# Performance work log

Measured on AMD Instinct MI355X. Metric: run time of the kernel, lower is better.

Reference implementation:

```python
import jax, jax.numpy as jnp
import numpy as np

B, T, Rn, D, O, E, H, C, TM = 20, 20, 20, 4096, 16, 512, 8, 68, 1900


def l2norm(x, axis=-1, eps=1e-12):
    return x / jnp.maximum(jnp.linalg.norm(x, axis=axis, keepdims=True), eps)


def setup_inputs() -> dict:
    key = jax.random.key(0)
    ks = jax.random.split(key, 10)
    return {
        "features": jax.random.normal(ks[0], (B, T, Rn, D), jnp.float32),
        "labels": jax.random.randint(ks[1], (B, O), 0, C),
        "temporal_mem": jax.random.normal(ks[2], (TM, T, D), jnp.float32),
        "entity_W": jax.random.normal(ks[3], (C, E), jnp.float32) / np.float32(np.sqrt(C)),
        "entity_b": jnp.zeros((E,), jnp.float32),
        "Wq": jax.random.normal(ks[4], (E, E), jnp.float32) / np.float32(np.sqrt(E)),
        "Wk": jax.random.normal(ks[5], (D, E), jnp.float32) / np.float32(np.sqrt(D)),
        "Wv": jax.random.normal(ks[6], (D, E), jnp.float32) / np.float32(np.sqrt(D)),
        "Wo": jax.random.normal(ks[7], (E, E), jnp.float32) / np.float32(np.sqrt(E)),
        "obj_W1": jax.random.normal(ks[8], (D, E), jnp.float32) / np.float32(np.sqrt(D)),
        "obj_b1": jnp.zeros((E,), jnp.float32),
        "obj_W2": jax.random.normal(ks[9], (E, 1), jnp.float32) / np.float32(np.sqrt(E)),
        "obj_b2": jnp.zeros((1,), jnp.float32),
    }


def reference(features, labels, temporal_mem, entity_W, entity_b, Wq, Wk, Wv, Wo,
              obj_W1, obj_b1, obj_W2, obj_b2):
    beta = 0.5   # loss mixing weight (module's beta)
    qgce = 0.7   # generalized-CE exponent
    Dh = E // H
    # region features, L2-normalized (dataset_feat == 'CVPR' path)
    Rf = l2norm(features)                                   # [B,T,Rn,D]

    # ---- temporal memory-bank kNN retrieval ----
    R_max = l2norm(jnp.max(Rf, axis=2))                     # [B,T,D] max-pool over regions
    mem_max = l2norm(jnp.max(temporal_mem, axis=1))         # [TM,D] max-pool over frames
    sim = jnp.einsum('btd,md->btm', R_max, mem_max)         # [B,T,TM]
    idx = jnp.argmax(sim, axis=-1)                          # [B,T] nearest memory slot
    Rp = temporal_mem[idx]                                  # [B,T,T,D] gathered memory videos
    mem_feat = jnp.max(Rp, axis=2)                          # [B,T,D]

    # ---- entity (object-label) embedding: one-hot with class 0 zeroed ----
    onehot = jax.nn.one_hot(labels, C, dtype=features.dtype)
    onehot = onehot * (labels != 0)[..., None].astype(features.dtype)
    Qe = onehot @ entity_W + entity_b                       # [B,O,E]

    # ---- multi-head attention fusion over regions + retrieved memory ----
    kv = jnp.concatenate([Rf.reshape(B, T * Rn, D), mem_feat], axis=1)  # [B,N,D]
    q = (Qe @ Wq).reshape(B, O, H, Dh)
    k = (kv @ Wk).reshape(B, -1, H, Dh)
    v = (kv @ Wv).reshape(B, -1, H, Dh)
    scores = jnp.einsum('bohd,bnhd->bhon', q, k) / np.float32(np.sqrt(Dh))
    attn = jax.nn.softmax(scores, axis=-1)
    fused = jnp.einsum('bhon,bnhd->bohd', attn, v).reshape(B, O, E) @ Wo  # [B,O,E]

    # ---- top-k region objectness selection + generalized CE ----
    QR = jax.lax.stop_gradient(jnp.mean(scores, axis=1)[:, :, :T * Rn].reshape(B, O, T, Rn))
    hi = jnp.argmax(QR, axis=-1)                            # [B,O,T] top-1 region
    lo = jnp.argmin(QR, axis=-1)                            # [B,O,T] low region
    bidx = jnp.arange(B)[:, None, None]
    tidx = jnp.arange(T)[None, None, :]
    R_high = Rf[bidx, tidx, hi]                             # [B,O,T,D]
    R_low = Rf[bidx, tidx, lo]                              # [B,O,T,D]
    osel = (labels != 0).astype(features.dtype)             # [B,O]
    onum = jnp.maximum(jnp.sum(osel, axis=1), 1.0)
    mlp = lambda x: jax.nn.sigmoid(jnp.tanh(x @ obj_W1 + obj_b1) @ obj_W2 + obj_b2)
    s_hi = mlp(R_high * osel[..., None, None]).squeeze(-1)  # [B,O,T]
    s_lo = mlp(R_low * osel[..., None, None]).squeeze(-1)
    gce_hi = jnp.mean((1.0 - (s_hi + 1e-7) ** qgce) / qgce * osel[..., None], axis=-1)
    gce_lo = jnp.mean((1.0 - (1.0 - s_lo + 1e-7) ** qgce) / qgce * osel[..., None], axis=-1)
    gce = jnp.mean(jnp.sum(gce_hi, axis=1) / onum) + jnp.mean(jnp.sum(gce_lo, axis=1) / onum)

    return fused + beta * gce
```

## Files before the change

kernel.cpp:

```cpp
#include <hip/hip_runtime.h>

#define B_   20
#define T_   20
#define RN   20
#define D_   4096
#define O_   16
#define E_   512
#define H_   8
#define DH   64
#define TM_  1900
#define MREG 8192
#define NW   1536
#define NSIM 2048
#define MSIM 512
#define CAP  256

using f32x4  = __attribute__((ext_vector_type(4))) float;
using bf16x8 = __attribute__((ext_vector_type(8))) __bf16;

__device__ __forceinline__ unsigned short f2bf(float f){
  unsigned u = __float_as_uint(f);
  u += 0x7fffu + ((u >> 16) & 1u);
  return (unsigned short)(u >> 16);
}

__device__ __forceinline__ void st_bf4(unsigned short* dst, float4 v){
  ushort4 o = make_ushort4(f2bf(v.x), f2bf(v.y), f2bf(v.z), f2bf(v.w));
  *(ushort4*)dst = o;
}

__device__ __forceinline__ float bsum256(float v, float* sh){
  int t = threadIdx.x;
  for (int o = 32; o; o >>= 1) v += __shfl_down(v, o, 64);
  __syncthreads();
  if ((t & 63) == 0) sh[t >> 6] = v;
  __syncthreads();
  return sh[0] + sh[1] + sh[2] + sh[3];
}

__device__ __forceinline__ float bmax256(float v, float* sh){
  int t = threadIdx.x;
  for (int o = 32; o; o >>= 1) v = fmaxf(v, __shfl_down(v, o, 64));
  __syncthreads();
  if ((t & 63) == 0) sh[t >> 6] = v;
  __syncthreads();
  return fmaxf(fmaxf(sh[0], sh[1]), fmaxf(sh[2], sh[3]));
}

__device__ __forceinline__ void gld16(const void* g, void* l){
  __builtin_amdgcn_global_load_lds(
      (const __attribute__((address_space(1))) unsigned int*)g,
      (__attribute__((address_space(3))) unsigned int*)l, 16, 0, 0);
}

__global__ __launch_bounds__(256) void k_pre(
    const float* __restrict__ F, const float* __restrict__ TMm,
    const float* __restrict__ Wk, const float* __restrict__ Wv, const float* __restrict__ W1,
    unsigned short* __restrict__ Wall,
    unsigned short* __restrict__ A, float* __restrict__ rmaxr, float* __restrict__ rmsum,
    unsigned short* __restrict__ ubf,
    float* __restrict__ umax, float* __restrict__ msum, unsigned short* __restrict__ gbf,
    const int* __restrict__ labels, const float* __restrict__ entW, const float* __restrict__ entB,
    const float* __restrict__ Wq, float* __restrict__ q){
  __shared__ char smem[4352];
  int bid = blockIdx.x, t = threadIdx.x;
  if (bid < 2048){
    int m = bid;
    if (m >= TM_){
      int4 zz = make_int4(0,0,0,0);
      int4* r2 = (int4*)(gbf + (size_t)m*D_);
      r2[t] = zz; r2[t + 256] = zz;
      return;
    }
    float* sh = (float*)smem;
    const float* base = TMm + (size_t)m*T_*D_;
    float4 mx[4];
#pragma unroll
    for (int i = 0; i < 4; ++i) mx[i] = make_float4(-1e30f,-1e30f,-1e30f,-1e30f);
    float4 va[2][4];
#pragma unroll
    for (int i = 0; i < 4; ++i) va[0][i] = *(const float4*)(base + i*1024 + t*4);
#pragma unroll
    for (int f = 0; f < T_; ++f){
      int c = f & 1;
      if (f + 1 < T_){
#pragma unroll
        for (int i = 0; i < 4; ++i)
          va[c^1][i] = *(const float4*)(base + (size_t)(f+1)*D_ + i*1024 + t*4);
      }
#pragma unroll
      for (int i = 0; i < 4; ++i){
        mx[i].x = fmaxf(mx[i].x, va[c][i].x); mx[i].y = fmaxf(mx[i].y, va[c][i].y);
        mx[i].z = fmaxf(mx[i].z, va[c][i].z); mx[i].w = fmaxf(mx[i].w, va[c][i].w);
      }
    }
    float s = 0.f;
#pragma unroll
    for (int i = 0; i < 4; ++i){
      *(float4*)(umax + (size_t)m*D_ + i*1024 + t*4) = mx[i];
      st_bf4(gbf + (size_t)m*D_ + i*1024 + t*4, mx[i]);
      s += mx[i].x*mx[i].x + mx[i].y*mx[i].y + mx[i].z*mx[i].z + mx[i].w*mx[i].w;
    }
    s = bsum256(s, sh);
    if (t == 0) msum[m] = s;
  } else if (bid < 2560){
    int bt = bid - 2048;
    if (bt >= 400){
      int4 zz = make_int4(0,0,0,0);
      int4* r1 = (int4*)(ubf + (size_t)bt*D_);
      r1[t] = zz; r1[t + 256] = zz;
      int base = 8000 + (bt - 400)*2;
#pragma unroll
      for (int k = 0; k < 2; ++k){
        if (base + k < MREG){
          int4* r2 = (int4*)(A + (size_t)(base + k)*D_);
          r2[t] = zz; r2[t + 256] = zz;
        }
      }
      return;
    }
    float* sh = (float*)smem;
    const float* fb = F + (size_t)bt*RN*D_;
    unsigned short* ab = A + (size_t)bt*RN*D_;
    float4 mx[4];
#pragma unroll
    for (int i = 0; i < 4; ++i) mx[i] = make_float4(-1e30f,-1e30f,-1e30f,-1e30f);
    float4 vn[4];
#pragma unroll
    for (int i = 0; i < 4; ++i) vn[i] = *(const float4*)(fb + i*1024 + t*4);
    for (int r = 0; r < RN; ++r){
      float4 v[4];
      float s = 0.f;
#pragma unroll
      for (int i = 0; i < 4; ++i){
        v[i] = vn[i];
        s += v[i].x*v[i].x + v[i].y*v[i].y + v[i].z*v[i].z + v[i].w*v[i].w;
      }
      if (r + 1 < RN){
#pragma unroll
        for (int i = 0; i < 4; ++i)
          vn[i] = *(const float4*)(fb + (size_t)(r+1)*D_ + i*1024 + t*4);
      }
      s = bsum256(s, sh);
      float ri = 1.f / fmaxf(sqrtf(s), 1e-12f);
#pragma unroll
      for (int i = 0; i < 4; ++i){
        v[i].x *= ri; v[i].y *= ri; v[i].z *= ri; v[i].w *= ri;
        st_bf4(ab + (size_t)r*D_ + i*1024 + t*4, v[i]);
        mx[i].x = fmaxf(mx[i].x, v[i].x); mx[i].y = fmaxf(mx[i].y, v[i].y);
        mx[i].z = fmaxf(mx[i].z, v[i].z); mx[i].w = fmaxf(mx[i].w, v[i].w);
      }
    }
    float s2 = 0.f;
#pragma unroll
    for (int i = 0; i < 4; ++i){
      *(float4*)(rmaxr + (size_t)bt*D_ + i*1024 + t*4) = mx[i];
      s2 += mx[i].x*mx[i].x + mx[i].y*mx[i].y + mx[i].z*mx[i].z + mx[i].w*mx[i].w;
    }
    s2 = bsum256(s2, sh);
    if (t == 0) rmsum[bt] = s2;
    float inv = 1.f / fmaxf(sqrtf(s2), 1e-12f);
#pragma unroll
    for (int i = 0; i < 4; ++i){
      float4 u = mx[i];
      u.x *= inv; u.y *= inv; u.z *= inv; u.w *= inv;
      st_bf4(ubf + (size_t)bt*D_ + i*1024 + t*4, u);
    }
  } else if (bid < 8704){
    int wti = bid - 2560;
    float* tile = (float*)smem;
    int kb = (wti & 127) * 32, nb = (wti >> 7) * 32;
    const float* src; int nc0;
    if (nb < 512)      { src = Wk; nc0 = nb; }
    else if (nb < 1024){ src = Wv; nc0 = nb - 512; }
    else               { src = W1; nc0 = nb - 1024; }
    int tx = t & 31, ty = t >> 5;
#pragma unroll
    for (int j = 0; j < 4; ++j){
      int k = kb + ty + j*8;
      tile[(ty + j*8)*33 + tx] = src[(size_t)k*E_ + nc0 + tx];
    }
    __syncthreads();
#pragma unroll
    for (int j = 0; j < 4; ++j){
      int n = nb + ty + j*8;
      int k = kb + tx;
      Wall[(size_t)n*D_ + k] = f2bf(tile[tx*33 + ty + j*8]);
    }
  } else {
    int bo = bid - 8704;
    float* qe = (float*)smem;
    int lab = labels[bo];
    float sel = (lab != 0) ? 1.f : 0.f;
    qe[t]       = sel * entW[(size_t)lab*E_ + t]       + entB[t];
    qe[t + 256] = sel * entW[(size_t)lab*E_ + t + 256] + entB[t + 256];
    __syncthreads();
    float a0 = 0.f, a1 = 0.f;
    for (int ep = 0; ep < E_; ++ep){
      float r = qe[ep];
      a0 += r * Wq[(size_t)ep*E_ + t];
      a1 += r * Wq[(size_t)ep*E_ + t + 256];
    }
    q[(size_t)bo*E_ + t] = a0;
    q[(size_t)bo*E_ + t + 256] = a1;
  }
}

__global__ __launch_bounds__(512, 1) void k_gemm3(
    const unsigned short* __restrict__ Akv, const unsigned short* __restrict__ Wall,
    const unsigned short* __restrict__ ubf, const unsigned short* __restrict__ gbf,
    float* __restrict__ C2, float* __restrict__ simc, float* __restrict__ Gc){
  __shared__ char lds[131072];
  int bid = blockIdx.x;
  bid = (bid & 7)*32 + (bid >> 3);
  const unsigned short *A, *Bw; float* C; int nNt, ldc, mt, nt;
  if (bid < 192){       A = Akv; Bw = Wall;  C = C2;   nNt = 6; ldc = NW;   mt = bid/6;  nt = bid%6; }
  else if (bid < 208){  int s = bid - 192;
                        A = ubf; Bw = gbf;   C = simc; nNt = 8; ldc = NSIM; mt = s/8;    nt = s%8; }
  else {                int s = bid - 208;
                        A = gbf; Bw = Wall;  C = Gc;   nNt = 6; ldc = NW;   mt = s/6;    nt = s%6; }
  int tid = threadIdx.x, wid = tid >> 6, l = tid & 63;
  int wr = (wid >> 2) * 128;
  int wc = (wid & 3) * 64;
  int fr = l & 15, fq = l >> 4;
  const char* Ab = (const char*)A + (size_t)mt*256*(size_t)(D_*2);
  const char* Bb = (const char*)Bw + (size_t)nt*256*(size_t)(D_*2);
  f32x4 acc[8][4];
#pragma unroll
  for (int m = 0; m < 8; ++m)
#pragma unroll
    for (int n = 0; n < 4; ++n) acc[m][n] = (f32x4){0.f,0.f,0.f,0.f};

#pragma unroll
  for (int i = 0; i < 4; ++i){
    int idx = i*512 + tid;
    int row = idx >> 3, u = idx & 7;
    int ul = u ^ (row & 7);
    gld16(Ab + (size_t)row*(D_*2) + (size_t)(ul*16), lds + idx*16);
    gld16(Bb + (size_t)row*(D_*2) + (size_t)(ul*16), lds + 32768 + idx*16);
  }
  __syncthreads();

  int c = 0;
  for (int kt = 0; kt < D_/64; ++kt){
    if (kt < D_/64 - 1){
      int ktoff = (kt + 1) * 128;
      char* dA = lds + (c^1)*65536;
      char* dB = dA + 32768;
#pragma unroll
      for (int i = 0; i < 4; ++i){
        int idx = i*512 + tid;
        int row = idx >> 3, u = idx & 7;
        int ul = u ^ (row & 7);
        gld16(Ab + (size_t)row*(D_*2) + ktoff + ul*16, dA + idx*16);
        gld16(Bb + (size_t)row*(D_*2) + ktoff + ul*16, dB + idx*16);
      }
    }
    const char* LA = lds + c*65536;
    const char* LB = LA + 32768;
    bf16x8 bv[4][2];
#pragma unroll
    for (int n = 0; n < 4; ++n)
#pragma unroll
      for (int kk = 0; kk < 2; ++kk){
        int row = wc + n*16 + fr;
        int u = (kk*4 + fq) ^ (row & 7);
        bv[n][kk] = *(const bf16x8*)(LB + row*128 + u*16);
      }
    __builtin_amdgcn_s_setprio(1);
#pragma unroll
    for (int mp = 0; mp < 4; ++mp){
      bf16x8 av[2][2];
#pragma unroll
      for (int mm = 0; mm < 2; ++mm)
#pragma unroll
        for (int kk = 0; kk < 2; ++kk){
          int row = wr + (mp*2 + mm)*16 + fr;
          int u = (kk*4 + fq) ^ (row & 7);
          av[mm][kk] = *(const bf16x8*)(LA + row*128 + u*16);
        }
#pragma unroll
      for (int mm = 0; mm < 2; ++mm)
#pragma unroll
        for (int n = 0; n < 4; ++n)
#pragma unroll
          for (int kk = 0; kk < 2; ++kk)
            acc[mp*2 + mm][n] = __builtin_amdgcn_mfma_f32_16x16x32_bf16(
                av[mm][kk], bv[n][kk], acc[mp*2 + mm][n], 0, 0, 0);
    }
    __builtin_amdgcn_s_setprio(0);
    __syncthreads();
    c ^= 1;
  }
  size_t crow0 = (size_t)mt*256 + wr, ccol0 = (size_t)nt*256 + wc;
#pragma unroll
  for (int m = 0; m < 8; ++m)
#pragma unroll
    for (int n = 0; n < 4; ++n){
      size_t r0 = crow0 + m*16 + fq*4, c0 = ccol0 + n*16 + fr;
#pragma unroll
      for (int j = 0; j < 4; ++j)
        C[(r0 + j)*(size_t)ldc + c0] = acc[m][n][j];
    }
}

__global__ __launch_bounds__(256) void k_pick(const float* __restrict__ simc,
                                              const float* __restrict__ rmaxr, const float* __restrict__ rmsum,
                                              const float* __restrict__ umax, const float* __restrict__ msum,
                                              const float* __restrict__ Gc, float* __restrict__ C2){
  int bt = blockIdx.x, t = threadIdx.x;
  __shared__ float srow[1920];
  __shared__ float sh[4];
  __shared__ int cnt;
  __shared__ int cl[CAP];
  for (int m = t; m < TM_; m += 256)
    srow[m] = simc[(size_t)bt*NSIM + m] * (1.f / fmaxf(sqrtf(msum[m]), 1e-12f));
  if (t == 0) cnt = 0;
  __syncthreads();
  float mx = -1e30f;
  for (int m = t; m < TM_; m += 256) mx = fmaxf(mx, srow[m]);
  mx = bmax256(mx, sh);
  float thr = mx - 2.5e-4f;
  for (int m = t; m < TM_; m += 256){
    if (srow[m] >= thr){
      int p = atomicAdd(&cnt, 1);
      if (p < CAP) cl[p] = m;
    }
  }
  __syncthreads();
  int cn = cnt < CAP ? cnt : CAP;
  float rinvv = 1.f / fmaxf(sqrtf(rmsum[bt]), 1e-12f);
  const float* a = rmaxr + (size_t)bt*D_;
  float best = -1e30f; int bestm = 0x7fffffff;
  for (int ci = 0; ci < cn; ++ci){
    int m = cl[ci];
    const float* wrow = umax + (size_t)m*D_;
    float p = 0.f;
    for (int i = t*4; i < D_; i += 1024){
      float4 av = *(const float4*)(a + i);
      float4 wv = *(const float4*)(wrow + i);
      p += av.x*wv.x + av.y*wv.y + av.z*wv.z + av.w*wv.w;
    }
    p = bsum256(p, sh);
    float sim = p * rinvv * (1.f / fmaxf(sqrtf(msum[m]), 1e-12f));
    if (sim > best || (sim == best && m < bestm)){ best = sim; bestm = m; }
  }
  const float4* src = (const float4*)(Gc + (size_t)bestm*NW);
  float4* dst = (float4*)(C2 + (size_t)(MREG + bt)*NW);
  if (t < 128){ dst[t] = src[t]; dst[t + 128] = src[t + 128]; dst[t + 256] = src[t + 256]; }
}

__global__ __launch_bounds__(256) void k_post(const float* __restrict__ q, const float* __restrict__ c2,
                                              float* __restrict__ fpre, int* __restrict__ hi,
                                              int* __restrict__ lo, const float* __restrict__ b1,
                                              const float* __restrict__ W2, const float* __restrict__ b2,
                                              float* __restrict__ z){
  __shared__ char smem[58368];
  int bid = blockIdx.x, t = threadIdx.x;
  if (bid < 160){
    int b = bid >> 3, h = bid & 7;
    int w = t >> 6, l = t & 63;
    float* qhp = (float*)smem;
    float* kb  = (float*)(smem + 4160);
    float* sc  = (float*)(smem + 31460);
    for (int i = t; i < O_*DH; i += 256){
      int o = i >> 6, d = i & 63;
      qhp[o*65 + d] = q[((size_t)(b*O_ + o))*E_ + h*DH + d] * 0.125f;
    }
    __syncthreads();
    for (int c = 0; c < 4; ++c){
      for (int i = t; i < 105*DH; i += 256){
        int j = i >> 6, d = i & 63;
        int n = c*105 + j;
        size_t row = n < 400 ? (size_t)b*400 + n : (size_t)MREG + b*20 + (n - 400);
        kb[j*65 + d] = c2[row*NW + h*DH + d];
      }
      __syncthreads();
      for (int i = t; i < O_*105; i += 256){
        int o = i / 105, j = i % 105;
        float acc = 0.f;
        for (int d = 0; d < DH; ++d) acc += qhp[o*65 + d] * kb[j*65 + d];
        sc[o*420 + c*105 + j] = acc;
      }
      __syncthreads();
    }
    for (int oi = 0; oi < 4; ++oi){
      int o = w + oi*4;
      float mxv = -1e30f;
      for (int n = l; n < 420; n += 64) mxv = fmaxf(mxv, sc[o*420 + n]);
      for (int of = 32; of; of >>= 1) mxv = fmaxf(mxv, __shfl_xor(mxv, of, 64));
      float sum = 0.f;
      for (int n = l; n < 420; n += 64){ float e = expf(sc[o*420 + n] - mxv); sc[o*420 + n] = e; sum += e; }
      for (int of = 32; of; of >>= 1) sum += __shfl_xor(sum, of, 64);
      float inv = 1.f / sum;
      for (int n = l; n < 420; n += 64) sc[o*420 + n] *= inv;
    }
    __syncthreads();
    float acc[4] = {0.f, 0.f, 0.f, 0.f};
    for (int c = 0; c < 4; ++c){
      for (int i = t; i < 105*DH; i += 256){
        int j = i >> 6, d = i & 63;
        int n = c*105 + j;
        size_t row = n < 400 ? (size_t)b*400 + n : (size_t)MREG + b*20 + (n - 400);
        kb[j*65 + d] = c2[row*NW + E_ + h*DH + d];
      }
      __syncthreads();
#pragma unroll
      for (int og = 0; og < 4; ++og){
        int o = og*4 + w;
        float a = 0.f;
        for (int j = 0; j < 105; ++j) a += sc[o*420 + c*105 + j] * kb[j*65 + l];
        acc[og] += a;
      }
      __syncthreads();
    }
#pragma unroll
    for (int og = 0; og < 4; ++og){
      int o = og*4 + w;
      fpre[((size_t)(b*O_ + o))*E_ + h*DH + l] = acc[og];
    }
  } else if (bid < 560){
    int bt = bid - 160;
    int b = bt / T_, tt = bt % T_;
    float* kl = (float*)smem;
    float* qr = (float*)(smem + 41040);
    for (int i = t; i < RN*E_; i += 256){
      int r = i >> 9, e = i & 511;
      kl[r*513 + e] = c2[((size_t)b*400 + tt*RN + r)*NW + e];
    }
    __syncthreads();
#pragma unroll
    for (int pp = 0; pp < 2; ++pp){
      int p = t + pp*256;
      if (p < O_*RN){
        int o = p / RN, r = p % RN;
        const float* qrow = q + ((size_t)(b*O_ + o))*E_;
        float acc = 0.f;
        for (int e = 0; e < E_; ++e) acc += qrow[e] * kl[r*513 + e];
        qr[o*20 + r] = acc;
      }
    }
    __syncthreads();
    if (t < O_){
      int o = t;
      float bh = qr[o*20], bl = qr[o*20]; int ih = 0, il = 0;
#pragma unroll
      for (int r = 1; r < RN; ++r){
        float v = qr[o*20 + r];
        if (v > bh){ bh = v; ih = r; }
        if (v < bl){ bl = v; il = r; }
      }
      int rowbase = b*400 + tt*RN;
      int outi = (b*O_ + o)*T_ + tt;
      hi[outi] = rowbase + ih;
      lo[outi] = rowbase + il;
    }
  } else {
    int g = (bid - 560)*4 + (t >> 6);
    int l = t & 63;
    const float* hrow = c2 + (size_t)g*NW + 1024;
    float acc = 0.f;
    for (int e = l; e < E_; e += 64) acc += tanhf(hrow[e] + b1[e]) * W2[e];
    for (int of = 32; of; of >>= 1) acc += __shfl_down(acc, of, 64);
    if (l == 0) z[g] = 1.f / (1.f + expf(-(acc + b2[0])));
  }
}

__global__ __launch_bounds__(256) void k_outg(const float* __restrict__ fpre, const float* __restrict__ Wo,
                                              const float* __restrict__ z, const int* __restrict__ hi,
                                              const int* __restrict__ lo, const int* __restrict__ labels,
                                              float* __restrict__ out){
  int bo = blockIdx.x, t = threadIdx.x;
  __shared__ float rowv[E_];
  __shared__ float vb[B_];
  __shared__ int cb[B_];
  __shared__ float gsh;
  rowv[t] = fpre[(size_t)bo*E_ + t];
  rowv[t + 256] = fpre[(size_t)bo*E_ + t + 256];
  if (t < B_){ vb[t] = 0.f; cb[t] = 0; }
  __syncthreads();
  for (int p = t; p < B_*O_; p += 256){
    int b = p / O_;
    if (labels[p] != 0){
      float acc = 0.f;
      for (int tt = 0; tt < T_; ++tt){
        float shi = z[hi[p*T_ + tt]];
        float slo = z[lo[p*T_ + tt]];
        acc += (1.f - __powf(shi + 1e-7f, 0.7f)) / 0.7f;
        acc += (1.f - __powf(1.f - slo + 1e-7f, 0.7f)) / 0.7f;
      }
      atomicAdd(&vb[b], acc / (float)T_);
      atomicAdd(&cb[b], 1);
    }
  }
  __syncthreads();
  if (t == 0){
    float g = 0.f;
    for (int b = 0; b < B_; ++b) g += vb[b] / fmaxf((float)cb[b], 1.f);
    gsh = 0.5f * (g / (float)B_);
  }
  __syncthreads();
  float g = gsh;
  float a0 = 0.f, a1 = 0.f;
  for (int ep = 0; ep < E_; ++ep){
    float r = rowv[ep];
    a0 += r * Wo[(size_t)ep*E_ + t];
    a1 += r * Wo[(size_t)ep*E_ + t + 256];
  }
  out[(size_t)bo*E_ + t] = a0 + g;
  out[(size_t)bo*E_ + t + 256] = a1 + g;
}

extern "C" void kernel_launch(void* const* d_in, const int* in_sizes, int n_in,
                              void* d_out, int out_size, void* d_ws, size_t ws_size,
                              hipStream_t stream) {
  (void)in_sizes; (void)n_in; (void)out_size; (void)ws_size;
  const float* F    = (const float*)d_in[0];
  const int*   labels = (const int*)d_in[1];
  const float* TMm  = (const float*)d_in[2];
  const float* entW = (const float*)d_in[3];
  const float* entB = (const float*)d_in[4];
  const float* Wq   = (const float*)d_in[5];
  const float* Wk   = (const float*)d_in[6];
  const float* Wv   = (const float*)d_in[7];
  const float* Wo   = (const float*)d_in[8];
  const float* W1   = (const float*)d_in[9];
  const float* b1   = (const float*)d_in[10];
  const float* W2   = (const float*)d_in[11];
  const float* b2   = (const float*)d_in[12];
  float* out = (float*)d_out;

  size_t off = 0;
  char* wsb = (char*)d_ws;
  auto alloc = [&](size_t bytes) -> char* {
    char* p = wsb + off; off += (bytes + 255) & ~(size_t)255; return p;
  };
  unsigned short* A_kv = (unsigned short*)alloc((size_t)MREG * D_ * 2);
  unsigned short* Wall = (unsigned short*)alloc((size_t)NW * D_ * 2);
  float* umax          = (float*)alloc((size_t)TM_ * D_ * 4);
  unsigned short* gbf  = (unsigned short*)alloc((size_t)NSIM * D_ * 2);
  unsigned short* ubf  = (unsigned short*)alloc((size_t)MSIM * D_ * 2);
  float* rmaxr = (float*)alloc((size_t)400 * D_ * 4);
  float* simc  = (float*)alloc((size_t)MSIM * NSIM * 4);
  float* Gc    = (float*)alloc((size_t)NSIM * NW * 4);
  float* C2    = (float*)alloc((size_t)(MREG + 512) * NW * 4);
  float* qbuf  = (float*)alloc((size_t)B_ * O_ * E_ * 4);
  float* fpre  = (float*)alloc((size_t)B_ * O_ * E_ * 4);
  float* rmsum = (float*)alloc(400 * 4);
  float* msum  = (float*)alloc(TM_ * 4);
  int*   hib   = (int*)alloc(6400 * 4);
  int*   lob   = (int*)alloc(6400 * 4);
  float* zbuf  = (float*)alloc(8000 * 4);

  k_pre<<<9024, 256, 0, stream>>>(F, TMm, Wk, Wv, W1, Wall, A_kv, rmaxr, rmsum, ubf,
                                  umax, msum, gbf, labels, entW, entB, Wq, qbuf);
  k_gemm3<<<256, 512, 0, stream>>>(A_kv, Wall, ubf, gbf, C2, simc, Gc);
  k_pick<<<400, 256, 0, stream>>>(simc, rmaxr, rmsum, umax, msum, Gc, C2);
  k_post<<<2560, 256, 0, stream>>>(qbuf, C2, fpre, hib, lob, b1, W2, b2, zbuf);
  k_outg<<<B_*O_, 256, 0, stream>>>(fpre, Wo, zbuf, hib, lob, labels, out);
}
```

Before: 487.0 us.

## Interleave next-tile global loads with MFMA phases in the GEMM main loop

Restructures the double-buffered bf16 GEMM loop so the prefetch of the next K tile is split into four quarter-stages, each issued alongside one of the four MFMA sub-phases. It replaces the single end-of-iteration __syncthreads with explicit vmcnt/lgkmcnt waits, s_barrier calls and sched_barriers around each phase. The aim is to spread memory issue across the compute and keep waves in lockstep so loads overlap with matrix math. In exchange it adds more barriers per iteration, and the hand-written waitcnt counts must match the number of outstanding loads exactly to avoid races.

```diff
diff --git a/kernel.cpp b/kernel.cpp
--- a/kernel.cpp
+++ b/kernel.cpp
@@ -231,66 +231,68 @@
 #pragma unroll
     for (int n = 0; n < 4; ++n) acc[m][n] = (f32x4){0.f,0.f,0.f,0.f};
 
-#pragma unroll
-  for (int i = 0; i < 4; ++i){
-    int idx = i*512 + tid;
-    int row = idx >> 3, u = idx & 7;
-    int ul = u ^ (row & 7);
-    gld16(Ab + (size_t)row*(D_*2) + (size_t)(ul*16), lds + idx*16);
-    gld16(Bb + (size_t)row*(D_*2) + (size_t)(ul*16), lds + 32768 + idx*16);
-  }
-  __syncthreads();
-
-  int c = 0;
+  auto stage_half = [&](char* dstbuf, int ktoff, int h){
+    const char* src = (h < 2) ? Ab : Bb;
+    int hh = h & 1;
+    char* dst = dstbuf + ((h < 2) ? 0 : 32768);
+#pragma unroll
+    for (int j = 0; j < 2; ++j){
+      int idx = (2*hh + j)*512 + tid;
+      int row = idx >> 3, u = idx & 7;
+      int ul = u ^ (row & 7);
+      gld16(src + (size_t)row*(size_t)(D_*2) + ktoff + ul*16, dst + idx*16);
+    }
+  };
+
+#pragma unroll
+  for (int h = 0; h < 4; ++h) stage_half(lds, 0, h);
+
   for (int kt = 0; kt < D_/64; ++kt){
-    if (kt < D_/64 - 1){
-      int ktoff = (kt + 1) * 128;
-      char* dA = lds + (c^1)*65536;
-      char* dB = dA + 32768;
-#pragma unroll
-      for (int i = 0; i < 4; ++i){
-        int idx = i*512 + tid;
-        int row = idx >> 3, u = idx & 7;
-        int ul = u ^ (row & 7);
-        gld16(Ab + (size_t)row*(D_*2) + ktoff + ul*16, dA + idx*16);
-        gld16(Bb + (size_t)row*(D_*2) + ktoff + ul*16, dB + idx*16);
-      }
-    }
-    const char* LA = lds + c*65536;
-    const char* LB = LA + 32768;
+    char* curb = lds + (kt & 1)*65536;
+    char* nxtb = lds + ((kt & 1)^1)*65536;
+    int nktoff = (kt + 1)*128;
     bf16x8 bv[4][2];
 #pragma unroll
-    for (int n = 0; n < 4; ++n)
-#pragma unroll
-      for (int kk = 0; kk < 2; ++kk){
-        int row = wc + n*16 + fr;
-        int u = (kk*4 + fq) ^ (row & 7);
-        bv[n][kk] = *(const bf16x8*)(LB + row*128 + u*16);
-      }
-    __builtin_amdgcn_s_setprio(1);
-#pragma unroll
-    for (int mp = 0; mp < 4; ++mp){
+    for (int p = 0; p < 4; ++p){
+      if (kt < D_/64 - 1) stage_half(nxtb, nktoff, p);
+      if (p == 0){
+        if (kt < D_/64 - 1) asm volatile("s_waitcnt vmcnt(2)" ::: "memory");
+        else                asm volatile("s_waitcnt vmcnt(0)" ::: "memory");
+        __builtin_amdgcn_s_barrier();
+        __builtin_amdgcn_sched_barrier(0);
+#pragma unroll
+        for (int n = 0; n < 4; ++n)
+#pragma unroll
+          for (int kk = 0; kk < 2; ++kk){
+            int row = wc + n*16 + fr;
+            int u = (kk*4 + fq) ^ (row & 7);
+            bv[n][kk] = *(const bf16x8*)(curb + 32768 + row*128 + u*16);
+          }
+      }
       bf16x8 av[2][2];
 #pragma unroll
       for (int mm = 0; mm < 2; ++mm)
 #pragma unroll
         for (int kk = 0; kk < 2; ++kk){
-          int row = wr + (mp*2 + mm)*16 + fr;
+          int row = wr + (p*2 + mm)*16 + fr;
           int u = (kk*4 + fq) ^ (row & 7);
-          av[mm][kk] = *(const bf16x8*)(LA + row*128 + u*16);
+          av[mm][kk] = *(const bf16x8*)(curb + row*128 + u*16);
         }
+      __builtin_amdgcn_s_barrier();
+      asm volatile("s_waitcnt lgkmcnt(0)" ::: "memory");
+      __builtin_amdgcn_sched_barrier(0);
+      __builtin_amdgcn_s_setprio(1);
 #pragma unroll
       for (int mm = 0; mm < 2; ++mm)
 #pragma unroll
         for (int n = 0; n < 4; ++n)
 #pragma unroll
           for (int kk = 0; kk < 2; ++kk)
-            acc[mp*2 + mm][n] = __builtin_amdgcn_mfma_f32_16x16x32_bf16(
-                av[mm][kk], bv[n][kk], acc[mp*2 + mm][n], 0, 0, 0);
-    }
-    __builtin_amdgcn_s_setprio(0);
-    __syncthreads();
-    c ^= 1;
+            acc[p*2 + mm][n] = __builtin_amdgcn_mfma_f32_16x16x32_bf16(
+                av[mm][kk], bv[n][kk], acc[p*2 + mm][n], 0, 0, 0);
+      __builtin_amdgcn_s_setprio(0);
+      __builtin_amdgcn_s_barrier();
+    }
   }
   size_t crow0 = (size_t)mt*256 + wr, ccol0 = (size_t)nt*256 + wc;
 #pragma unroll
```

After: 488.4 us. About the same (+0.3%).

## Overlap memory-bank max-pool with main GEMM and split-K the sim/Gc GEMMs

Applied to the files above, without the earlier changes.

Moves the temporal-memory max-pool out of the preprocessing kernel and runs it in the same launch as the main K/V/W1 GEMM tiles, so the bandwidth-bound reduction can overlap with the compute-bound GEMM. The similarity and memory-projection GEMMs move into a separate kernel and use split-K (8 and 4 partitions). This fills more blocks and shortens the serial K loop, and the picking kernel sums the partials. The Gc projection shrinks to 1024 columns. The cost is more partial-sum traffic and an extra launch.

```diff
diff --git a/kernel.cpp b/kernel.cpp
--- a/kernel.cpp
+++ b/kernel.cpp
@@ -13,7 +13,10 @@
 #define NW   1536
 #define NSIM 2048
 #define MSIM 512
+#define NG   1024
 #define CAP  256
+#define SIMK 8
+#define GK   4
 
 using f32x4  = __attribute__((ext_vector_type(4))) float;
 using bf16x8 = __attribute__((ext_vector_type(8))) __bf16;
@@ -53,58 +56,18 @@
       (__attribute__((address_space(3))) unsigned int*)l, 16, 0, 0);
 }
 
-__global__ __launch_bounds__(256) void k_pre(
-    const float* __restrict__ F, const float* __restrict__ TMm,
+__global__ __launch_bounds__(256) void k_prelight(
+    const float* __restrict__ F,
     const float* __restrict__ Wk, const float* __restrict__ Wv, const float* __restrict__ W1,
     unsigned short* __restrict__ Wall,
     unsigned short* __restrict__ A, float* __restrict__ rmaxr, float* __restrict__ rmsum,
     unsigned short* __restrict__ ubf,
-    float* __restrict__ umax, float* __restrict__ msum, unsigned short* __restrict__ gbf,
     const int* __restrict__ labels, const float* __restrict__ entW, const float* __restrict__ entB,
     const float* __restrict__ Wq, float* __restrict__ q){
   __shared__ char smem[4352];
   int bid = blockIdx.x, t = threadIdx.x;
-  if (bid < 2048){
-    int m = bid;
-    if (m >= TM_){
-      int4 zz = make_int4(0,0,0,0);
-      int4* r2 = (int4*)(gbf + (size_t)m*D_);
-      r2[t] = zz; r2[t + 256] = zz;
-      return;
-    }
-    float* sh = (float*)smem;
-    const float* base = TMm + (size_t)m*T_*D_;
-    float4 mx[4];
-#pragma unroll
-    for (int i = 0; i < 4; ++i) mx[i] = make_float4(-1e30f,-1e30f,-1e30f,-1e30f);
-    float4 va[2][4];
-#pragma unroll
-    for (int i = 0; i < 4; ++i) va[0][i] = *(const float4*)(base + i*1024 + t*4);
-#pragma unroll
-    for (int f = 0; f < T_; ++f){
-      int c = f & 1;
-      if (f + 1 < T_){
-#pragma unroll
-        for (int i = 0; i < 4; ++i)
-          va[c^1][i] = *(const float4*)(base + (size_t)(f+1)*D_ + i*1024 + t*4);
-      }
-#pragma unroll
-      for (int i = 0; i < 4; ++i){
-        mx[i].x = fmaxf(mx[i].x, va[c][i].x); mx[i].y = fmaxf(mx[i].y, va[c][i].y);
-        mx[i].z = fmaxf(mx[i].z, va[c][i].z); mx[i].w = fmaxf(mx[i].w, va[c][i].w);
-      }
-    }
-    float s = 0.f;
-#pragma unroll
-    for (int i = 0; i < 4; ++i){
-      *(float4*)(umax + (size_t)m*D_ + i*1024 + t*4) = mx[i];
-      st_bf4(gbf + (size_t)m*D_ + i*1024 + t*4, mx[i]);
-      s += mx[i].x*mx[i].x + mx[i].y*mx[i].y + mx[i].z*mx[i].z + mx[i].w*mx[i].w;
-    }
-    s = bsum256(s, sh);
-    if (t == 0) msum[m] = s;
-  } else if (bid < 2560){
-    int bt = bid - 2048;
+  if (bid < 512){
+    int bt = bid;
     if (bt >= 400){
       int4 zz = make_int4(0,0,0,0);
       int4* r1 = (int4*)(ubf + (size_t)bt*D_);
@@ -166,8 +129,8 @@
       u.x *= inv; u.y *= inv; u.z *= inv; u.w *= inv;
       st_bf4(ubf + (size_t)bt*D_ + i*1024 + t*4, u);
     }
-  } else if (bid < 8704){
-    int wti = bid - 2560;
+  } else if (bid < 6656){
+    int wti = bid - 512;
     float* tile = (float*)smem;
     int kb = (wti & 127) * 32, nb = (wti >> 7) * 32;
     const float* src; int nc0;
@@ -188,7 +151,7 @@
       Wall[(size_t)n*D_ + k] = f2bf(tile[tx*33 + ty + j*8]);
     }
   } else {
-    int bo = bid - 8704;
+    int bo = bid - 6656;
     float* qe = (float*)smem;
     int lab = labels[bo];
     float sel = (lab != 0) ? 1.f : 0.f;
@@ -206,19 +169,164 @@
   }
 }
 
-__global__ __launch_bounds__(512, 1) void k_gemm3(
+__global__ __launch_bounds__(512, 1) void k_mix(
     const unsigned short* __restrict__ Akv, const unsigned short* __restrict__ Wall,
+    float* __restrict__ C2,
+    const float* __restrict__ TMm, float* __restrict__ umax, float* __restrict__ msum,
+    unsigned short* __restrict__ gbf){
+  __shared__ char lds[131072];
+  int bid = blockIdx.x, t = threadIdx.x;
+  if (bid < 192){
+    int sb = (bid & 7)*24 + (bid >> 3);
+    int mt = sb / 6, nt = sb % 6;
+    int tid = t, wid = tid >> 6, l = tid & 63;
+    int wr = (wid >> 2) * 128;
+    int wc = (wid & 3) * 64;
+    int fr = l & 15, fq = l >> 4;
+    const char* Ab = (const char*)Akv + (size_t)mt*256*(size_t)(D_*2);
+    const char* Bb = (const char*)Wall + (size_t)nt*256*(size_t)(D_*2);
+    f32x4 acc[8][4];
+#pragma unroll
+    for (int m = 0; m < 8; ++m)
+#pragma unroll
+      for (int n = 0; n < 4; ++n) acc[m][n] = (f32x4){0.f,0.f,0.f,0.f};
+#pragma unroll
+    for (int i = 0; i < 4; ++i){
+      int idx = i*512 + tid;
+      int row = idx >> 3, u = idx & 7;
+      int ul = u ^ (row & 7);
+      gld16(Ab + (size_t)row*(D_*2) + (size_t)(ul*16), lds + idx*16);
+      gld16(Bb + (size_t)row*(D_*2) + (size_t)(ul*16), lds + 32768 + idx*16);
+    }
+    __syncthreads();
+    int c = 0;
+    for (int kt = 0; kt < D_/64; ++kt){
+      if (kt < D_/64 - 1){
+        int ktoff = (kt + 1) * 128;
+        char* dA = lds + (c^1)*65536;
+        char* dB = dA + 32768;
+#pragma unroll
+        for (int i = 0; i < 4; ++i){
+          int idx = i*512 + tid;
+          int row = idx >> 3, u = idx & 7;
+          int ul = u ^ (row & 7);
+          gld16(Ab + (size_t)row*(D_*2) + ktoff + ul*16, dA + idx*16);
+          gld16(Bb + (size_t)row*(D_*2) + ktoff + ul*16, dB + idx*16);
+        }
+      }
+      const char* LA = lds + c*65536;
+      const char* LB = LA + 32768;
+      bf16x8 bv[4][2];
+#pragma unroll
+      for (int n = 0; n < 4; ++n)
+#pragma unroll
+        for (int kk = 0; kk < 2; ++kk){
+          int row = wc + n*16 + fr;
+          int u = (kk*4 + fq) ^ (row & 7);
+          bv[n][kk] = *(const bf16x8*)(LB + row*128 + u*16);
+        }
+      __builtin_amdgcn_s_setprio(1);
+#pragma unroll
+      for (int mp = 0; mp < 4; ++mp){
+        bf16x8 av[2][2];
+#pragma unroll
+        for (int mm = 0; mm < 2; ++mm)
+#pragma unroll
+          for (int kk = 0; kk < 2; ++kk){
+            int row = wr + (mp*2 + mm)*16 + fr;
+            int u = (kk*4 + fq) ^ (row & 7);
+            av[mm][kk] = *(const bf16x8*)(LA + row*128 + u*16);
+          }
+#pragma unroll
+        for (int mm = 0; mm < 2; ++mm)
+#pragma unroll
+          for (int n = 0; n < 4; ++n)
+#pragma unroll
+            for (int kk = 0; kk < 2; ++kk)
+              acc[mp*2 + mm][n] = __builtin_amdgcn_mfma_f32_16x16x32_bf16(
+                  av[mm][kk], bv[n][kk], acc[mp*2 + mm][n], 0, 0, 0);
+      }
+      __builtin_amdgcn_s_setprio(0);
+      __syncthreads();
+      c ^= 1;
+    }
+    size_t crow0 = (size_t)mt*256 + wr, ccol0 = (size_t)nt*256 + wc;
+#pragma unroll
+    for (int m = 0; m < 8; ++m)
+#pragma unroll
+      for (int n = 0; n < 4; ++n){
+        size_t r0 = crow0 + m*16 + fq*4, c0 = ccol0 + n*16 + fr;
+#pragma unroll
+        for (int j = 0; j < 4; ++j)
+          C2[(r0 + j)*(size_t)NW + c0] = acc[m][n][j];
+      }
+  } else {
+    int m = bid - 192;
+    if (m >= TM_){
+      int4 zz = make_int4(0,0,0,0);
+      ((int4*)(gbf + (size_t)m*D_))[t] = zz;
+      return;
+    }
+    float* sh = (float*)lds;
+    const float* base = TMm + (size_t)m*T_*D_;
+    float4 mx[2];
+#pragma unroll
+    for (int i = 0; i < 2; ++i) mx[i] = make_float4(-1e30f,-1e30f,-1e30f,-1e30f);
+    float4 va[2][2];
+#pragma unroll
+    for (int i = 0; i < 2; ++i) va[0][i] = *(const float4*)(base + i*2048 + t*4);
+#pragma unroll
+    for (int f = 0; f < T_; ++f){
+      int c = f & 1;
+      if (f + 1 < T_){
+#pragma unroll
+        for (int i = 0; i < 2; ++i)
+          va[c^1][i] = *(const float4*)(base + (size_t)(f+1)*D_ + i*2048 + t*4);
+      }
+#pragma unroll
+      for (int i = 0; i < 2; ++i){
+        mx[i].x = fmaxf(mx[i].x, va[c][i].x); mx[i].y = fmaxf(mx[i].y, va[c][i].y);
+        mx[i].z = fmaxf(mx[i].z, va[c][i].z); mx[i].w = fmaxf(mx[i].w, va[c][i].w);
+      }
+    }
+    float s = 0.f;
+#pragma unroll
+    for (int i = 0; i < 2; ++i){
+      *(float4*)(umax + (size_t)m*D_ + i*2048 + t*4) = mx[i];
+      st_bf4(gbf + (size_t)m*D_ + i*2048 + t*4, mx[i]);
+      s += mx[i].x*mx[i].x + mx[i].y*mx[i].y + mx[i].z*mx[i].z + mx[i].w*mx[i].w;
+    }
+    for (int o = 32; o; o >>= 1) s += __shfl_down(s, o, 64);
+    __syncthreads();
+    if ((t & 63) == 0) sh[t >> 6] = s;
+    __syncthreads();
+    if (t == 0){
+      float tot = 0.f;
+#pragma unroll
+      for (int w = 0; w < 8; ++w) tot += sh[w];
+      msum[m] = tot;
+    }
+  }
+}
+
+__global__ __launch_bounds__(512, 1) void k_simg(
     const unsigned short* __restrict__ ubf, const unsigned short* __restrict__ gbf,
-    float* __restrict__ C2, float* __restrict__ simc, float* __restrict__ Gc){
+    const unsigned short* __restrict__ Wall,
+    float* __restrict__ simp, float* __restrict__ Gcp){
   __shared__ char lds[131072];
   int bid = blockIdx.x;
   bid = (bid & 7)*32 + (bid >> 3);
-  const unsigned short *A, *Bw; float* C; int nNt, ldc, mt, nt;
-  if (bid < 192){       A = Akv; Bw = Wall;  C = C2;   nNt = 6; ldc = NW;   mt = bid/6;  nt = bid%6; }
-  else if (bid < 208){  int s = bid - 192;
-                        A = ubf; Bw = gbf;   C = simc; nNt = 8; ldc = NSIM; mt = s/8;    nt = s%8; }
-  else {                int s = bid - 208;
-                        A = gbf; Bw = Wall;  C = Gc;   nNt = 6; ldc = NW;   mt = s/6;    nt = s%6; }
+  const unsigned short *A, *Bw; float* C; int ldc, mt, nt, kt0, nkt;
+  if (bid < 128){
+    int p = bid >> 4, s = bid & 15;
+    A = ubf; Bw = gbf; C = simp + (size_t)p*MSIM*NSIM; ldc = NSIM;
+    mt = s >> 3; nt = s & 7; kt0 = p*(64/SIMK); nkt = 64/SIMK;
+  } else {
+    int s2 = bid - 128;
+    int p = s2 >> 5, idx = s2 & 31;
+    A = gbf; Bw = Wall; C = Gcp + (size_t)p*NSIM*NG; ldc = NG;
+    mt = idx >> 2; nt = idx & 3; kt0 = p*(64/GK); nkt = 64/GK;
+  }
   int tid = threadIdx.x, wid = tid >> 6, l = tid & 63;
   int wr = (wid >> 2) * 128;
   int wc = (wid & 3) * 64;
@@ -230,20 +338,18 @@
   for (int m = 0; m < 8; ++m)
 #pragma unroll
     for (int n = 0; n < 4; ++n) acc[m][n] = (f32x4){0.f,0.f,0.f,0.f};
-
 #pragma unroll
   for (int i = 0; i < 4; ++i){
     int idx = i*512 + tid;
     int row = idx >> 3, u = idx & 7;
     int ul = u ^ (row & 7);
-    gld16(Ab + (size_t)row*(D_*2) + (size_t)(ul*16), lds + idx*16);
-    gld16(Bb + (size_t)row*(D_*2) + (size_t)(ul*16), lds + 32768 + idx*16);
-  }
-  __syncthreads();
-
+    gld16(Ab + (size_t)row*(D_*2) + (size_t)(kt0*128 + ul*16), lds + idx*16);
+    gld16(Bb + (size_t)row*(D_*2) + (size_t)(kt0*128 + ul*16), lds + 32768 + idx*16);
+  }
+  __syncthreads();
   int c = 0;
-  for (int kt = 0; kt < D_/64; ++kt){
-    if (kt < D_/64 - 1){
+  for (int kt = kt0; kt < kt0 + nkt; ++kt){
+    if (kt < kt0 + nkt - 1){
       int ktoff = (kt + 1) * 128;
       char* dA = lds + (c^1)*65536;
       char* dB = dA + 32768;
@@ -304,17 +410,22 @@
     }
 }
 
-__global__ __launch_bounds__(256) void k_pick(const float* __restrict__ simc,
+__global__ __launch_bounds__(256) void k_pick(const float* __restrict__ simp,
                                               const float* __restrict__ rmaxr, const float* __restrict__ rmsum,
                                               const float* __restrict__ umax, const float* __restrict__ msum,
-                                              const float* __restrict__ Gc, float* __restrict__ C2){
+                                              const float* __restrict__ Gcp, float* __restrict__ C2){
   int bt = blockIdx.x, t = threadIdx.x;
   __shared__ float srow[1920];
   __shared__ float sh[4];
   __shared__ int cnt;
   __shared__ int cl[CAP];
-  for (int m = t; m < TM_; m += 256)
-    srow[m] = simc[(size_t)bt*NSIM + m] * (1.f / fmaxf(sqrtf(msum[m]), 1e-12f));
+  for (int m = t; m < TM_; m += 256){
+    float s = 0.f;
+#pragma unroll
+    for (int p = 0; p < SIMK; ++p)
+      s += simp[(size_t)p*MSIM*NSIM + (size_t)bt*NSIM + m];
+    srow[m] = s * (1.f / fmaxf(sqrtf(msum[m]), 1e-12f));
+  }
   if (t == 0) cnt = 0;
   __syncthreads();
   float mx = -1e30f;
@@ -345,9 +456,15 @@
     float sim = p * rinvv * (1.f / fmaxf(sqrtf(msum[m]), 1e-12f));
     if (sim > best || (sim == best && m < bestm)){ best = sim; bestm = m; }
   }
-  const float4* src = (const float4*)(Gc + (size_t)bestm*NW);
-  float4* dst = (float4*)(C2 + (size_t)(MREG + bt)*NW);
-  if (t < 128){ dst[t] = src[t]; dst[t + 128] = src[t + 128]; dst[t + 256] = src[t + 256]; }
+  float* dst = C2 + (size_t)(MREG + bt)*NW;
+  int j = t*4;
+  float4 accv = make_float4(0.f,0.f,0.f,0.f);
+#pragma unroll
+  for (int p = 0; p < GK; ++p){
+    float4 v = *(const float4*)(Gcp + (size_t)p*NSIM*NG + (size_t)bestm*NG + j);
+    accv.x += v.x; accv.y += v.y; accv.z += v.z; accv.w += v.w;
+  }
+  *(float4*)(dst + j) = accv;
 }
 
 __global__ __launch_bounds__(256) void k_post(const float* __restrict__ q, const float* __restrict__ c2,
@@ -541,8 +658,8 @@
   unsigned short* gbf  = (unsigned short*)alloc((size_t)NSIM * D_ * 2);
   unsigned short* ubf  = (unsigned short*)alloc((size_t)MSIM * D_ * 2);
   float* rmaxr = (float*)alloc((size_t)400 * D_ * 4);
-  float* simc  = (float*)alloc((size_t)MSIM * NSIM * 4);
-  float* Gc    = (float*)alloc((size_t)NSIM * NW * 4);
+  float* simp  = (float*)alloc((size_t)SIMK * MSIM * NSIM * 4);
+  float* Gcp   = (float*)alloc((size_t)GK * NSIM * NG * 4);
   float* C2    = (float*)alloc((size_t)(MREG + 512) * NW * 4);
   float* qbuf  = (float*)alloc((size_t)B_ * O_ * E_ * 4);
   float* fpre  = (float*)alloc((size_t)B_ * O_ * E_ * 4);
@@ -552,10 +669,11 @@
   int*   lob   = (int*)alloc(6400 * 4);
   float* zbuf  = (float*)alloc(8000 * 4);
 
-  k_pre<<<9024, 256, 0, stream>>>(F, TMm, Wk, Wv, W1, Wall, A_kv, rmaxr, rmsum, ubf,
-                                  umax, msum, gbf, labels, entW, entB, Wq, qbuf);
-  k_gemm3<<<256, 512, 0, stream>>>(A_kv, Wall, ubf, gbf, C2, simc, Gc);
-  k_pick<<<400, 256, 0, stream>>>(simc, rmaxr, rmsum, umax, msum, Gc, C2);
+  k_prelight<<<6976, 256, 0, stream>>>(F, Wk, Wv, W1, Wall, A_kv, rmaxr, rmsum, ubf,
+                                       labels, entW, entB, Wq, qbuf);
+  k_mix<<<2240, 512, 0, stream>>>(A_kv, Wall, C2, TMm, umax, msum, gbf);
+  k_simg<<<256, 512, 0, stream>>>(ubf, gbf, Wall, simp, Gcp);
+  k_pick<<<400, 256, 0, stream>>>(simp, rmaxr, rmsum, umax, msum, Gcp, C2);
   k_post<<<2560, 256, 0, stream>>>(qbuf, C2, fpre, hib, lob, b1, W2, b2, zbuf);
   k_outg<<<B_*O_, 256, 0, stream>>>(fpre, Wo, zbuf, hib, lob, labels, out);
 }
```

New measurement: 494.3 us. No clear change (+1.5%).
